# Optimization experiments

Hardware: AMD Instinct MI355X
Metric: run time of the kernel (lower is better)

The kernel has to match this reference:

```python
import jax, jax.numpy as jnp
import numpy as np

L, NH, D, FF, NL, NP = 6, 8, 256, 1024, 4, 4
HD = D // NH
B, Q0 = 4, 1000
SIZES = [(128, 128), (64, 64), (32, 32), (16, 16)]
KEEP_RATIO = 0.5


def _ln(x, w, b, eps=1e-5):
    mu = x.mean(-1, keepdims=True)
    var = ((x - mu) ** 2).mean(-1, keepdims=True)
    return (x - mu) * jax.lax.rsqrt(var + eps) * w + b


def _mha(q, k, v, in_w, in_b, out_w, out_b):
    # torch nn.MultiheadAttention (batch_first, eval mode => no dropout)
    Bq, Qn, _ = q.shape
    wq, wk, wv = jnp.split(in_w, 3, axis=0)
    bq, bk, bv = jnp.split(in_b, 3, axis=0)
    proj = lambda x, w, bb: (x @ w.T + bb).reshape(Bq, -1, NH, HD).transpose(0, 2, 1, 3)
    qh, kh, vh = proj(q, wq, bq), proj(k, wk, bk), proj(v, wv, bv)
    scores = jnp.einsum('bhqd,bhkd->bhqk', qh, kh) * (1.0 / np.float32(np.sqrt(HD)))
    a = jax.nn.softmax(scores, axis=-1)
    o = jnp.einsum('bhqk,bhkd->bhqd', a, vh).transpose(0, 2, 1, 3).reshape(Bq, Qn, D)
    return o @ out_w.T + out_b


def _bilinear(feat, grid):
    # feat [B,NH,HD,H,W]; grid [B,NH,Q,P,2] (x,y) in [-1,1]
    # matches F.grid_sample(mode='bilinear', padding_mode='zeros', align_corners=True)
    Bf, nh, hd, H, W = feat.shape
    gx = (grid[..., 0] + 1.0) * 0.5 * (W - 1)
    gy = (grid[..., 1] + 1.0) * 0.5 * (H - 1)
    x0, y0 = jnp.floor(gx), jnp.floor(gy)
    flat = feat.reshape(Bf, nh, hd, H * W)
    Qn, P = grid.shape[2], grid.shape[3]

    def corner(xi, yi, w):
        valid = (xi >= 0) & (xi <= W - 1) & (yi >= 0) & (yi <= H - 1)
        idx = (jnp.clip(yi, 0, H - 1).astype(jnp.int32) * W
               + jnp.clip(xi, 0, W - 1).astype(jnp.int32)).reshape(Bf, nh, Qn * P)
        vals = jnp.take_along_axis(flat, jnp.broadcast_to(idx[:, :, None, :], (Bf, nh, hd, Qn * P)), axis=3)
        vals = vals.reshape(Bf, nh, hd, Qn, P)
        return vals * (w * valid)[:, :, None]

    wx1, wy1 = gx - x0, gy - y0
    return (corner(x0, y0, (1 - wx1) * (1 - wy1)) + corner(x0 + 1, y0, wx1 * (1 - wy1))
            + corner(x0, y0 + 1, (1 - wx1) * wy1) + corner(x0 + 1, y0 + 1, wx1 * wy1))


def _msdeform(query, feats, ref, off_w, off_b, aw_w, aw_b, out_w, out_b):
    Bq, Qn, _ = query.shape
    off = jnp.tanh((query @ off_w.T + off_b).reshape(Bq, Qn, NH, NL, NP, 2))
    attn = jax.nn.softmax((query @ aw_w.T + aw_b).reshape(Bq, Qn, NH, NL * NP), axis=3)
    attn = attn.reshape(Bq, Qn, NH, NL, NP)
    ref_grid = ref * 2.0 - 1.0  # [B,Q,2]
    agg = 0.0
    for lvl, feat in enumerate(feats):
        fh = feat.reshape(Bq, NH, HD, feat.shape[2], feat.shape[3])
        grid = ref_grid[:, None, :, None, :] + off[:, :, :, lvl].transpose(0, 2, 1, 3, 4)  # [B,NH,Q,NP,2]
        sampled = _bilinear(fh, grid)                     # [B,NH,HD,Q,NP]
        w = attn[:, :, :, lvl].transpose(0, 2, 1, 3)      # [B,NH,Q,NP]
        agg = agg + (sampled * w[:, :, None]).sum(-1)     # [B,NH,HD,Q]
    out = agg.transpose(0, 3, 1, 2).reshape(Bq, Qn, D)
    return out @ out_w.T + out_b, attn


def setup_inputs() -> dict:
    key = jax.random.key(0)
    ks = iter(jax.random.split(key, 64))
    nrm = lambda shape, s=0.02: jax.random.normal(next(ks), shape, jnp.float32) * s
    inp = {
        'query_objects': nrm((B, Q0, D), 1.0),
        'query_embed': nrm((B, Q0, D), 1.0),
    }
    for i, (H, W) in enumerate(SIZES):
        inp[f'feat{i}'] = nrm((B, D, H, W), 1.0)
    inp.update(
        sa_in_w=nrm((L, 3 * D, D)), sa_in_b=jnp.zeros((L, 3 * D)),
        sa_out_w=nrm((L, D, D)), sa_out_b=jnp.zeros((L, D)),
        off_w=nrm((L, NH * NL * NP * 2, D)), off_b=nrm((L, NH * NL * NP * 2), 0.1),
        aw_w=nrm((L, NH * NL * NP, D)), aw_b=jnp.zeros((L, NH * NL * NP)),
        ca_out_w=nrm((L, D, D)), ca_out_b=jnp.zeros((L, D)),
        ff_w1=nrm((L, FF, D)), ff_b1=jnp.zeros((L, FF)),
        ff_w2=nrm((L, D, FF)), ff_b2=jnp.zeros((L, D)),
        nsa_w=jnp.ones((L, D)), nsa_b=jnp.zeros((L, D)),
        nca_w=jnp.ones((L, D)), nca_b=jnp.zeros((L, D)),
        nff_w=jnp.ones((L, D)), nff_b=jnp.zeros((L, D)),
        ref_w1=nrm((D, D)), ref_b1=jnp.zeros((D,)),
        ref_w2=nrm((2, D)), ref_b2=jnp.zeros((2,)),
        score_w=nrm((1, D)), score_b=jnp.zeros((1,)),
        refine_w=nrm((2, D)), refine_b=jnp.zeros((2,)),
    )
    return inp


def reference(query_objects, query_embed, feat0, feat1, feat2, feat3,
              sa_in_w, sa_in_b, sa_out_w, sa_out_b,
              off_w, off_b, aw_w, aw_b, ca_out_w, ca_out_b,
              ff_w1, ff_b1, ff_w2, ff_b2,
              nsa_w, nsa_b, nca_w, nca_b, nff_w, nff_b,
              ref_w1, ref_b1, ref_w2, ref_b2,
              score_w, score_b, refine_w, refine_b):
    feats = [feat0, feat1, feat2, feat3]
    out, q_embed = query_objects, query_embed
    h = jax.nn.relu(q_embed @ ref_w1.T + ref_b1)
    ref_points = jax.nn.sigmoid(h @ ref_w2.T + ref_b2)  # [B,Q,2]
    outputs, attns = [], []
    for i in range(L):
        sa_in = _ln(out, nsa_w[i], nsa_b[i])
        sa_out = _mha(sa_in + q_embed, sa_in + q_embed, sa_in,
                      sa_in_w[i], sa_in_b[i], sa_out_w[i], sa_out_b[i])
        out = out + sa_out
        ca_in = _ln(out, nca_w[i], nca_b[i])
        ca_out, attn = _msdeform(ca_in + q_embed, feats, ref_points,
                                 off_w[i], off_b[i], aw_w[i], aw_b[i], ca_out_w[i], ca_out_b[i])
        out = out + ca_out
        ff_in = _ln(out, nff_w[i], nff_b[i])
        out = out + (jax.nn.relu(ff_in @ ff_w1[i].T + ff_b1[i]) @ ff_w2[i].T + ff_b2[i])
        delta = jnp.tanh(out @ refine_w.T + refine_b) * 0.5
        ref_points = jnp.clip(ref_points + delta, 0.0, 1.0)
        outputs.append(out)
        attns.append(attn)
        if i < L - 1:
            Qn = out.shape[1]
            keep = max(16, int(Qn * KEEP_RATIO))
            scores = jax.nn.sigmoid((jax.lax.stop_gradient(out) @ score_w.T + score_b)[..., 0])
            _, idx = jax.lax.top_k(scores, keep)
            out = jnp.take_along_axis(out, idx[:, :, None], axis=1)
            q_embed = jnp.take_along_axis(q_embed, idx[:, :, None], axis=1)
            ref_points = jnp.take_along_axis(ref_points, idx[:, :, None], axis=1)
    return tuple(outputs) + tuple(attns)
```

## Files before the change

### kernel.cpp

```cpp
#include <hip/hip_runtime.h>
#include <hip/hip_bf16.h>

#define BB 4
#define DD 256

typedef unsigned long long u64;
typedef long long s64;
typedef unsigned int u32;

__device__ __forceinline__ float sigm(float x) { return 1.0f / (1.0f + expf(-x)); }

__global__ void k_ln(const float* __restrict__ x, const float* __restrict__ w,
                     const float* __restrict__ b, float* __restrict__ ln) {
    int row = blockIdx.x, tid = threadIdx.x;
    float v = x[(size_t)row * DD + tid];
    __shared__ float sred[4];
    float s = v;
#pragma unroll
    for (int o = 32; o > 0; o >>= 1) s += __shfl_down(s, o);
    if ((tid & 63) == 0) sred[tid >> 6] = s;
    __syncthreads();
    float mu = (sred[0] + sred[1] + sred[2] + sred[3]) * (1.0f / 256.0f);
    __syncthreads();
    float d = v - mu;
    float s2 = d * d;
#pragma unroll
    for (int o = 32; o > 0; o >>= 1) s2 += __shfl_down(s2, o);
    if ((tid & 63) == 0) sred[tid >> 6] = s2;
    __syncthreads();
    float var = (sred[0] + sred[1] + sred[2] + sred[3]) * (1.0f / 256.0f);
    float r = rsqrtf(var + 1e-5f);
    ln[(size_t)row * DD + tid] = d * r * w[tid] + b[tid];
}

template <int ACT, int RES>
__device__ __forceinline__ void gemm_core(float (*As)[16][64], float (*Ws)[16][64],
                                          const float* __restrict__ A, const float* __restrict__ Pe, int pe,
                                          const float* __restrict__ W, const float* __restrict__ bias,
                                          const float* __restrict__ Rm, float* __restrict__ C,
                                          float* __restrict__ C2,
                                          int M, int N, int K, int row0, int col0) {
    int tid = threadIdx.x;
    int tx = tid & 15, ty = tid >> 4;
    int lm = tid >> 2, lk = (tid & 3) * 4;
    float acc[4][4] = {{0.f}};
    int ar = row0 + lm;
    const float* Arow = A + (size_t)ar * K + lk;
    const float* Prow = pe ? (Pe + (size_t)ar * K + lk) : nullptr;
    const float* Wrow = W + (size_t)(col0 + lm) * K + lk;
    float4 av = make_float4(0.f, 0.f, 0.f, 0.f), wv;
    if (ar < M) {
        av = *(const float4*)(Arow);
        if (pe) { float4 pv = *(const float4*)(Prow); av.x += pv.x; av.y += pv.y; av.z += pv.z; av.w += pv.w; }
    }
    wv = *(const float4*)(Wrow);
    As[0][lk + 0][lm] = av.x; As[0][lk + 1][lm] = av.y; As[0][lk + 2][lm] = av.z; As[0][lk + 3][lm] = av.w;
    Ws[0][lk + 0][lm] = wv.x; Ws[0][lk + 1][lm] = wv.y; Ws[0][lk + 2][lm] = wv.z; Ws[0][lk + 3][lm] = wv.w;
    __syncthreads();
    int nb = K >> 4;
    for (int t = 0; t < nb; t++) {
        int cur = t & 1, nxt = cur ^ 1;
        bool more = (t + 1 < nb);
        if (more) {
            int k0 = (t + 1) << 4;
            av = make_float4(0.f, 0.f, 0.f, 0.f);
            if (ar < M) {
                av = *(const float4*)(Arow + k0);
                if (pe) { float4 pv = *(const float4*)(Prow + k0); av.x += pv.x; av.y += pv.y; av.z += pv.z; av.w += pv.w; }
            }
            wv = *(const float4*)(Wrow + k0);
        }
#pragma unroll
        for (int kk = 0; kk < 16; kk++) {
            float4 a = *(const float4*)&As[cur][kk][ty << 2];
            float4 w = *(const float4*)&Ws[cur][kk][tx << 2];
            acc[0][0] += a.x * w.x; acc[0][1] += a.x * w.y; acc[0][2] += a.x * w.z; acc[0][3] += a.x * w.w;
            acc[1][0] += a.y * w.x; acc[1][1] += a.y * w.y; acc[1][2] += a.y * w.z; acc[1][3] += a.y * w.w;
            acc[2][0] += a.z * w.x; acc[2][1] += a.z * w.y; acc[2][2] += a.z * w.z; acc[2][3] += a.z * w.w;
            acc[3][0] += a.w * w.x; acc[3][1] += a.w * w.y; acc[3][2] += a.w * w.z; acc[3][3] += a.w * w.w;
        }
        if (more) {
            As[nxt][lk + 0][lm] = av.x; As[nxt][lk + 1][lm] = av.y; As[nxt][lk + 2][lm] = av.z; As[nxt][lk + 3][lm] = av.w;
            Ws[nxt][lk + 0][lm] = wv.x; Ws[nxt][lk + 1][lm] = wv.y; Ws[nxt][lk + 2][lm] = wv.z; Ws[nxt][lk + 3][lm] = wv.w;
        }
        __syncthreads();
    }
#pragma unroll
    for (int i2 = 0; i2 < 4; i2++) {
        int r = row0 + (ty << 2) + i2;
        if (r >= M) continue;
        int cc = col0 + (tx << 2);
        float4 v;
        v.x = acc[i2][0] + bias[cc + 0];
        v.y = acc[i2][1] + bias[cc + 1];
        v.z = acc[i2][2] + bias[cc + 2];
        v.w = acc[i2][3] + bias[cc + 3];
        if (ACT == 1) { v.x = fmaxf(v.x, 0.f); v.y = fmaxf(v.y, 0.f); v.z = fmaxf(v.z, 0.f); v.w = fmaxf(v.w, 0.f); }
        if (RES == 1) {
            float4 rm = *(const float4*)(Rm + (size_t)r * N + cc);
            v.x += rm.x; v.y += rm.y; v.z += rm.z; v.w += rm.w;
        }
        *(float4*)(C + (size_t)r * N + cc) = v;
        if (C2) *(float4*)(C2 + (size_t)r * N + cc) = v;
    }
}

template <int ACT, int RES, int PE>
__global__ __launch_bounds__(256) void k_gemm(const float* __restrict__ A, const float* __restrict__ Pe,
                                              const float* __restrict__ W, const float* __restrict__ bias,
                                              const float* __restrict__ Rm, float* __restrict__ C,
                                              int M, int N, int K) {
    __shared__ float As[2][16][64];
    __shared__ float Ws[2][16][64];
    gemm_core<ACT, RES>(As, Ws, A, Pe, PE, W, bias, Rm, C, nullptr, M, N, K, blockIdx.y * 64, blockIdx.x * 64);
}

__global__ __launch_bounds__(256) void k_gemm_st2(const float* __restrict__ A, const float* __restrict__ W,
                                                  const float* __restrict__ bias, const float* __restrict__ Rm,
                                                  float* __restrict__ C, float* __restrict__ C2,
                                                  int M, int N, int K) {
    __shared__ float As[2][16][64];
    __shared__ float Ws[2][16][64];
    gemm_core<0, 1>(As, Ws, A, nullptr, 0, W, bias, Rm, C, C2, M, N, K, blockIdx.y * 64, blockIdx.x * 64);
}

__global__ __launch_bounds__(256) void k_gemm_qkv(const float* __restrict__ A, const float* __restrict__ Pe,
                                                  const float* __restrict__ Wqkv, const float* __restrict__ bqkv,
                                                  float* __restrict__ Cq, float* __restrict__ Ck, float* __restrict__ Cv,
                                                  int M, int K) {
    __shared__ float As[2][16][64];
    __shared__ float Ws[2][16][64];
    int z = blockIdx.z;
    const float* W = Wqkv + (size_t)z * 256 * K;
    const float* bias = bqkv + z * 256;
    float* C = (z == 0) ? Cq : (z == 1) ? Ck : Cv;
    gemm_core<0, 0>(As, Ws, A, Pe, (z < 2) ? 1 : 0, W, bias, nullptr, C, nullptr, M, 256, K,
                    blockIdx.y * 64, blockIdx.x * 64);
}

__global__ __launch_bounds__(256) void k_gemm_offaw(const float* __restrict__ A, const float* __restrict__ Pe,
                                                    const float* __restrict__ Woff, const float* __restrict__ boff,
                                                    const float* __restrict__ Waw, const float* __restrict__ baw,
                                                    float* __restrict__ Coff, float* __restrict__ Caw,
                                                    int M, int K) {
    __shared__ float As[2][16][64];
    __shared__ float Ws[2][16][64];
    int z = blockIdx.z;
    int N = (z == 0) ? 256 : 128;
    if ((int)(blockIdx.x * 64) >= N) return;
    gemm_core<0, 0>(As, Ws, A, Pe, 1, (z == 0) ? Woff : Waw, (z == 0) ? boff : baw, nullptr,
                    (z == 0) ? Coff : Caw, nullptr, M, N, K, blockIdx.y * 64, blockIdx.x * 64);
}

#define MHA_DOT8(SREG, JJ)                                                       \
    {                                                                            \
        _Pragma("unroll")                                                        \
        for (int u = 0; u < 8; u++) SREG[u] = 0.f;                               \
        _Pragma("unroll")                                                        \
        for (int c4 = 0; c4 < 8; c4++) {                                         \
            float q0 = qv[c4 * 4 + 0], q1 = qv[c4 * 4 + 1];                      \
            float q2 = qv[c4 * 4 + 2], q3 = qv[c4 * 4 + 3];                      \
            _Pragma("unroll")                                                    \
            for (int u = 0; u < 8; u++) {                                        \
                float4 k4 = *(const float4*)&Ks[(JJ) + u][c4 * 4];               \
                SREG[u] += q0 * k4.x; SREG[u] += q1 * k4.y;                      \
                SREG[u] += q2 * k4.z; SREG[u] += q3 * k4.w;                      \
            }                                                                    \
        }                                                                        \
    }

__global__ __launch_bounds__(64) void k_qk(const float* __restrict__ Qb, const float* __restrict__ Kb,
                                           float* __restrict__ S, int Qn) {
    int bh = blockIdx.z;
    int b = bh >> 3, h = bh & 7;
    int lane = threadIdx.x;
    int qi = blockIdx.x * 64 + lane;
    int j0 = blockIdx.y * 64;
    __shared__ float Ks[64][36];
    float qv[32];
    const float scale = 0.17677669529663687f;
    bool active = qi < Qn;
    if (active) {
        const float4* qp = (const float4*)(Qb + ((size_t)(b * Qn + qi)) * DD + h * 32);
#pragma unroll
        for (int c4 = 0; c4 < 8; c4++) {
            float4 t = qp[c4];
            qv[c4 * 4 + 0] = t.x * scale; qv[c4 * 4 + 1] = t.y * scale;
            qv[c4 * 4 + 2] = t.z * scale; qv[c4 * 4 + 3] = t.w * scale;
        }
    } else {
#pragma unroll
        for (int c = 0; c < 32; c++) qv[c] = 0.f;
    }
    int nj = Qn - j0; if (nj > 64) nj = 64;
    if (lane < nj) {
        const float4* kp = (const float4*)(Kb + ((size_t)(b * Qn + j0 + lane)) * DD + h * 32);
#pragma unroll
        for (int c4 = 0; c4 < 8; c4++) *(float4*)&Ks[lane][c4 * 4] = kp[c4];
    }
    __syncthreads();
    float* Sp = S + (size_t)bh * Qn * Qn;
    float scur[8];
    for (int g = 0; g < 8; g++) {
        int jj = g << 3;
        if (jj >= nj) break;
        MHA_DOT8(scur, jj)
#pragma unroll
        for (int u = 0; u < 8; u++) {
            int j = j0 + jj + u;
            if (active && j < Qn) Sp[(size_t)j * Qn + qi] = scur[u];
        }
    }
}

__global__ __launch_bounds__(64) void k_mha_s(const float* __restrict__ S, const float* __restrict__ Vb,
                                              float* __restrict__ Ob, int Qn) {
    int bh = blockIdx.y;
    int b = bh >> 3, h = bh & 7;
    int lane = threadIdx.x;
    int qi = blockIdx.x * 64 + lane;
    __shared__ float Vs[64][36];
    float acc[32];
#pragma unroll
    for (int c = 0; c < 32; c++) acc[c] = 0.f;
    float m = -INFINITY, l = 0.f;
    bool active = qi < Qn;
    int qs = active ? qi : 0;
    const float* Sq = S + (size_t)bh * Qn * Qn + qs;
    int ng = Qn >> 3;
    float scur[8], snxt[8];
#pragma unroll
    for (int u = 0; u < 8; u++) scur[u] = Sq[(size_t)u * Qn];
    int gg = 0;
    for (int k0 = 0; k0 < Qn; k0 += 64) {
        int nk = Qn - k0; if (nk > 64) nk = 64;
        if (lane < nk) {
            const float4* vp = (const float4*)(Vb + ((size_t)(b * Qn + k0 + lane)) * DD + h * 32);
#pragma unroll
            for (int c4 = 0; c4 < 8; c4++) *(float4*)&Vs[lane][c4 * 4] = vp[c4];
        }
        __syncthreads();
        int gl = nk >> 3;
        for (int g2 = 0; g2 < gl; g2++, gg++) {
            int jj = g2 << 3;
            bool morep = (gg + 1 < ng);
            if (morep) {
                const float* Sn = Sq + (size_t)(k0 + jj + 8) * Qn;
#pragma unroll
                for (int u = 0; u < 8; u++) snxt[u] = Sn[(size_t)u * Qn];
            }
            float mch[9];
            mch[0] = m;
#pragma unroll
            for (int u = 0; u < 8; u++) mch[u + 1] = fmaxf(mch[u], scur[u]);
            float e8[8];
#pragma unroll
            for (int u = 0; u < 8; u++) e8[u] = expf(fminf(mch[u] - scur[u], scur[u] - mch[u]));
            float sc8[8], p8[8];
#pragma unroll
            for (int u = 0; u < 8; u++) {
                bool gt = scur[u] > mch[u];
                sc8[u] = gt ? e8[u] : 1.0f;
                p8[u] = gt ? 1.0f : e8[u];
                l = l * sc8[u] + p8[u];
            }
            m = mch[8];
            float4 vc[8], vn[8];
#pragma unroll
            for (int c4 = 0; c4 < 8; c4++) vc[c4] = *(const float4*)&Vs[jj][c4 * 4];
#pragma unroll
            for (int u = 0; u < 8; u++) {
                if (u < 7) {
#pragma unroll
                    for (int c4 = 0; c4 < 8; c4++) vn[c4] = *(const float4*)&Vs[jj + u + 1][c4 * 4];
                }
                float sc = sc8[u], p = p8[u];
#pragma unroll
                for (int c4 = 0; c4 < 8; c4++) {
                    acc[c4 * 4 + 0] = acc[c4 * 4 + 0] * sc + p * vc[c4].x;
                    acc[c4 * 4 + 1] = acc[c4 * 4 + 1] * sc + p * vc[c4].y;
                    acc[c4 * 4 + 2] = acc[c4 * 4 + 2] * sc + p * vc[c4].z;
                    acc[c4 * 4 + 3] = acc[c4 * 4 + 3] * sc + p * vc[c4].w;
                }
                if (u < 7) {
#pragma unroll
                    for (int c4 = 0; c4 < 8; c4++) vc[c4] = vn[c4];
                }
            }
            if (morep) {
#pragma unroll
                for (int u = 0; u < 8; u++) scur[u] = snxt[u];
            }
        }
        for (int j = gl << 3; j < nk; j++) {
            float sv = Sq[(size_t)(k0 + j) * Qn];
            float mn = fmaxf(m, sv);
            float e = expf(fminf(m - sv, sv - m));
            bool gt = sv > m;
            float sc = gt ? e : 1.0f;
            float p = gt ? 1.0f : e;
            l = l * sc + p;
            m = mn;
#pragma unroll
            for (int c4 = 0; c4 < 8; c4++) {
                float4 v4 = *(const float4*)&Vs[j][c4 * 4];
                acc[c4 * 4 + 0] = acc[c4 * 4 + 0] * sc + p * v4.x;
                acc[c4 * 4 + 1] = acc[c4 * 4 + 1] * sc + p * v4.y;
                acc[c4 * 4 + 2] = acc[c4 * 4 + 2] * sc + p * v4.z;
                acc[c4 * 4 + 3] = acc[c4 * 4 + 3] * sc + p * v4.w;
            }
        }
        __syncthreads();
    }
    if (active) {
        float inv = 1.0f / l;
        float* op = Ob + ((size_t)(b * Qn + qi)) * DD + h * 32;
#pragma unroll
        for (int c4 = 0; c4 < 8; c4++) {
            float4 o;
            o.x = acc[c4 * 4 + 0] * inv; o.y = acc[c4 * 4 + 1] * inv;
            o.z = acc[c4 * 4 + 2] * inv; o.w = acc[c4 * 4 + 3] * inv;
            *(float4*)(op + c4 * 4) = o;
        }
    }
}

__global__ __launch_bounds__(64) void k_mha(const float* __restrict__ Qb, const float* __restrict__ Kb,
                                            const float* __restrict__ Vb, float* __restrict__ Ob, int Qn) {
    int bh = blockIdx.y;
    int b = bh >> 3, h = bh & 7;
    int lane = threadIdx.x;
    int qi = blockIdx.x * 64 + lane;
    __shared__ float Ks[64][36];
    __shared__ float Vs[64][36];
    float qv[32];
    float acc[32];
#pragma unroll
    for (int c = 0; c < 32; c++) acc[c] = 0.f;
    float m = -INFINITY, l = 0.f;
    const float scale = 0.17677669529663687f;
    bool active = qi < Qn;
    if (active) {
        const float4* qp = (const float4*)(Qb + ((size_t)(b * Qn + qi)) * DD + h * 32);
#pragma unroll
        for (int c4 = 0; c4 < 8; c4++) {
            float4 t = qp[c4];
            qv[c4 * 4 + 0] = t.x * scale; qv[c4 * 4 + 1] = t.y * scale;
            qv[c4 * 4 + 2] = t.z * scale; qv[c4 * 4 + 3] = t.w * scale;
        }
    } else {
#pragma unroll
        for (int c = 0; c < 32; c++) qv[c] = 0.f;
    }
    for (int k0 = 0; k0 < Qn; k0 += 64) {
        int nk = Qn - k0; if (nk > 64) nk = 64;
        if (lane < nk) {
            const float4* kp = (const float4*)(Kb + ((size_t)(b * Qn + k0 + lane)) * DD + h * 32);
            const float4* vp = (const float4*)(Vb + ((size_t)(b * Qn + k0 + lane)) * DD + h * 32);
#pragma unroll
            for (int c4 = 0; c4 < 8; c4++) {
                *(float4*)&Ks[lane][c4 * 4] = kp[c4];
                *(float4*)&Vs[lane][c4 * 4] = vp[c4];
            }
        }
        __syncthreads();
        int ng = nk >> 3;
        float scur[8], snxt[8];
        if (ng > 0) MHA_DOT8(scur, 0)
        for (int g = 0; g < ng; g++) {
            int jj = g << 3;
            bool morep = (g + 1 < ng);
            if (morep) MHA_DOT8(snxt, jj + 8)
            float mch[9];
            mch[0] = m;
#pragma unroll
            for (int u = 0; u < 8; u++) mch[u + 1] = fmaxf(mch[u], scur[u]);
            float e8[8];
#pragma unroll
            for (int u = 0; u < 8; u++) e8[u] = expf(fminf(mch[u] - scur[u], scur[u] - mch[u]));
            float sc8[8], p8[8];
#pragma unroll
            for (int u = 0; u < 8; u++) {
                bool gt = scur[u] > mch[u];
                sc8[u] = gt ? e8[u] : 1.0f;
                p8[u] = gt ? 1.0f : e8[u];
                l = l * sc8[u] + p8[u];
            }
            m = mch[8];
            float4 vc[8], vn[8];
#pragma unroll
            for (int c4 = 0; c4 < 8; c4++) vc[c4] = *(const float4*)&Vs[jj][c4 * 4];
#pragma unroll
            for (int u = 0; u < 8; u++) {
                if (u < 7) {
#pragma unroll
                    for (int c4 = 0; c4 < 8; c4++) vn[c4] = *(const float4*)&Vs[jj + u + 1][c4 * 4];
                }
                float sc = sc8[u], p = p8[u];
#pragma unroll
                for (int c4 = 0; c4 < 8; c4++) {
                    acc[c4 * 4 + 0] = acc[c4 * 4 + 0] * sc + p * vc[c4].x;
                    acc[c4 * 4 + 1] = acc[c4 * 4 + 1] * sc + p * vc[c4].y;
                    acc[c4 * 4 + 2] = acc[c4 * 4 + 2] * sc + p * vc[c4].z;
                    acc[c4 * 4 + 3] = acc[c4 * 4 + 3] * sc + p * vc[c4].w;
                }
                if (u < 7) {
#pragma unroll
                    for (int c4 = 0; c4 < 8; c4++) vc[c4] = vn[c4];
                }
            }
            if (morep) {
#pragma unroll
                for (int u = 0; u < 8; u++) scur[u] = snxt[u];
            }
        }
        for (int j = ng << 3; j < nk; j++) {
            float sv = 0.f;
#pragma unroll
            for (int c4 = 0; c4 < 8; c4++) {
                float4 k4 = *(const float4*)&Ks[j][c4 * 4];
                sv += qv[c4 * 4 + 0] * k4.x; sv += qv[c4 * 4 + 1] * k4.y;
                sv += qv[c4 * 4 + 2] * k4.z; sv += qv[c4 * 4 + 3] * k4.w;
            }
            float mn = fmaxf(m, sv);
            float e = expf(fminf(m - sv, sv - m));
            bool gt = sv > m;
            float sc = gt ? e : 1.0f;
            float p = gt ? 1.0f : e;
            l = l * sc + p;
            m = mn;
#pragma unroll
            for (int c4 = 0; c4 < 8; c4++) {
                float4 v4 = *(const float4*)&Vs[j][c4 * 4];
                acc[c4 * 4 + 0] = acc[c4 * 4 + 0] * sc + p * v4.x;
                acc[c4 * 4 + 1] = acc[c4 * 4 + 1] * sc + p * v4.y;
                acc[c4 * 4 + 2] = acc[c4 * 4 + 2] * sc + p * v4.z;
                acc[c4 * 4 + 3] = acc[c4 * 4 + 3] * sc + p * v4.w;
            }
        }
        __syncthreads();
    }
    if (active) {
        float inv = 1.0f / l;
        float* op = Ob + ((size_t)(b * Qn + qi)) * DD + h * 32;
#pragma unroll
        for (int c4 = 0; c4 < 8; c4++) {
            float4 o;
            o.x = acc[c4 * 4 + 0] * inv; o.y = acc[c4 * 4 + 1] * inv;
            o.z = acc[c4 * 4 + 2] * inv; o.w = acc[c4 * 4 + 3] * inv;
            *(float4*)(op + c4 * 4) = o;
        }
    }
}

__global__ __launch_bounds__(256) void k_trfeat(const float* __restrict__ in, float* __restrict__ out, int HH) {
    __shared__ float t[32][65];
    int bh = blockIdx.y;
    int b = bh >> 3, h = bh & 7;
    int s0 = blockIdx.x * 64;
    int tid = threadIdx.x;
    const float* ip = in + ((size_t)(b * 256 + h * 32)) * HH + s0;
#pragma unroll
    for (int i = 0; i < 8; i++) {
        int idx = i * 256 + tid;
        int c = idx >> 6, s = idx & 63;
        t[c][s] = ip[(size_t)c * HH + s];
    }
    __syncthreads();
    float* op = out + ((size_t)bh * HH + s0) * 32;
#pragma unroll
    for (int i = 0; i < 8; i++) {
        int idx = i * 256 + tid;
        int s = idx >> 5, c = idx & 31;
        op[(size_t)s * 32 + c] = t[c][s];
    }
}

__device__ __forceinline__ float d_samp(const float* fp, int W, int H, int x, int y) {
    if (x < 0 || x > W - 1 || y < 0 || y > H - 1) return 0.f;
    return fp[y * W + x];
}
__device__ __forceinline__ float d_bil(const float* fp, int W, int H, float gx, float gy) {
    float fx = (gx + 1.0f) * 0.5f * (float)(W - 1);
    float fy = (gy + 1.0f) * 0.5f * (float)(H - 1);
    float x0f = floorf(fx), y0f = floorf(fy);
    int x0 = (int)x0f, y0 = (int)y0f;
    float wx = fx - x0f, wy = fy - y0f;
    float v00 = d_samp(fp, W, H, x0, y0);
    float v10 = d_samp(fp, W, H, x0 + 1, y0);
    float v01 = d_samp(fp, W, H, x0, y0 + 1);
    float v11 = d_samp(fp, W, H, x0 + 1, y0 + 1);
    return v00 * (1.f - wx) * (1.f - wy) + v10 * wx * (1.f - wy) + v01 * (1.f - wx) * wy + v11 * wx * wy;
}
__device__ __forceinline__ float d_samp32(const float* fp, int W, int H, int x, int y) {
    if (x < 0 || x > W - 1 || y < 0 || y > H - 1) return 0.f;
    return fp[(size_t)(y * W + x) * 32];
}
__device__ __forceinline__ float d_bil32(const float* fp, int W, int H, float gx, float gy) {
    float fx = (gx + 1.0f) * 0.5f * (float)(W - 1);
    float fy = (gy + 1.0f) * 0.5f * (float)(H - 1);
    float x0f = floorf(fx), y0f = floorf(fy);
    int x0 = (int)x0f, y0 = (int)y0f;
    float wx = fx - x0f, wy = fy - y0f;
    float v00 = d_samp32(fp, W, H, x0, y0);
    float v10 = d_samp32(fp, W, H, x0 + 1, y0);
    float v01 = d_samp32(fp, W, H, x0, y0 + 1);
    float v11 = d_samp32(fp, W, H, x0 + 1, y0 + 1);
    return v00 * (1.f - wx) * (1.f - wy) + v10 * wx * (1.f - wy) + v01 * (1.f - wx) * wy + v11 * wx * wy;
}

template <int TR>
__global__ __launch_bounds__(256) void k_deform(const float* __restrict__ offL, const float* __restrict__ awL,
                                                const float* __restrict__ ref,
                                                const float* __restrict__ f0, const float* __restrict__ f1,
                                                const float* __restrict__ f2, const float* __restrict__ f3,
                                                float* __restrict__ caf, float* __restrict__ attn_out,
                                                int Qn) {
    int row = blockIdx.x;
    int b = row / Qn;
    int tid = threadIdx.x;
    __shared__ float attn_s[8][16];
    __shared__ float off_s[8][16][2];
    __shared__ float rxy[2];
    if (tid < 8) {
        int h = tid;
        const float* ap = awL + (size_t)row * 128 + h * 16;
        float mx = -INFINITY;
        float e[16];
#pragma unroll
        for (int j = 0; j < 16; j++) mx = fmaxf(mx, ap[j]);
        float ssum = 0.f;
#pragma unroll
        for (int j = 0; j < 16; j++) { e[j] = expf(ap[j] - mx); ssum += e[j]; }
        float inv = 1.0f / ssum;
        float* ao = attn_out + (size_t)row * 128 + h * 16;
#pragma unroll
        for (int j = 0; j < 16; j++) {
            float p = e[j] * inv;
            attn_s[h][j] = p;
            ao[j] = p;
        }
        const float* op = offL + (size_t)row * 256 + h * 32;
#pragma unroll
        for (int j = 0; j < 16; j++) {
            off_s[h][j][0] = tanhf(op[j * 2 + 0]);
            off_s[h][j][1] = tanhf(op[j * 2 + 1]);
        }
    }
    if (tid == 8) {
        rxy[0] = ref[(size_t)row * 2 + 0] * 2.f - 1.f;
        rxy[1] = ref[(size_t)row * 2 + 1] * 2.f - 1.f;
    }
    __syncthreads();
    int h = tid >> 5, c = tid & 31;
    float agg = 0.f;
#pragma unroll
    for (int l = 0; l < 4; l++) {
        const int H = 128 >> l;
        const float* base = (l == 0 ? f0 : l == 1 ? f1 : l == 2 ? f2 : f3);
        const float* fp;
        if (TR) fp = base + ((size_t)(b * 8 + h) * (H * H)) * 32 + c;
        else    fp = base + (size_t)(b * DD + h * 32 + c) * H * H;
#pragma unroll
        for (int p = 0; p < 4; p++) {
            int j = l * 4 + p;
            float sv;
            if (TR) sv = d_bil32(fp, H, H, rxy[0] + off_s[h][j][0], rxy[1] + off_s[h][j][1]);
            else    sv = d_bil(fp, H, H, rxy[0] + off_s[h][j][0], rxy[1] + off_s[h][j][1]);
            agg += attn_s[h][j] * sv;
        }
    }
    caf[(size_t)row * DD + h * 32 + c] = agg;
}

__global__ __launch_bounds__(64) void k_refinit(const float* __restrict__ hbuf, const float* __restrict__ w2,
                                                const float* __restrict__ b2, float* __restrict__ ref) {
    int row = blockIdx.x, lane = threadIdx.x;
    const float* hp = hbuf + (size_t)row * DD;
    float s0 = 0.f, s1 = 0.f;
#pragma unroll
    for (int d = 0; d < 4; d++) {
        int dd = lane + d * 64;
        float v = hp[dd];
        s0 += v * w2[dd];
        s1 += v * w2[DD + dd];
    }
#pragma unroll
    for (int o = 32; o > 0; o >>= 1) { s0 += __shfl_down(s0, o); s1 += __shfl_down(s1, o); }
    if (lane == 0) {
        ref[(size_t)row * 2 + 0] = sigm(s0 + b2[0]);
        ref[(size_t)row * 2 + 1] = sigm(s1 + b2[1]);
    }
}

__global__ __launch_bounds__(64) void k_refsc(const float* __restrict__ out, const float* __restrict__ rw,
                                              const float* __restrict__ rb, float* __restrict__ ref,
                                              const float* __restrict__ sw, const float* __restrict__ sb,
                                              float* __restrict__ score) {
    int row = blockIdx.x, lane = threadIdx.x;
    const float* op = out + (size_t)row * DD;
    float s0 = 0.f, s1 = 0.f;
#pragma unroll
    for (int d = 0; d < 4; d++) {
        int dd = lane + d * 64;
        float v = op[dd];
        s0 += v * rw[dd];
        s1 += v * rw[DD + dd];
    }
#pragma unroll
    for (int o = 32; o > 0; o >>= 1) { s0 += __shfl_down(s0, o); s1 += __shfl_down(s1, o); }
    if (lane == 0) {
        float r0 = ref[(size_t)row * 2 + 0] + tanhf(s0 + rb[0]) * 0.5f;
        float r1 = ref[(size_t)row * 2 + 1] + tanhf(s1 + rb[1]) * 0.5f;
        ref[(size_t)row * 2 + 0] = fminf(fmaxf(r0, 0.f), 1.f);
        ref[(size_t)row * 2 + 1] = fminf(fmaxf(r1, 0.f), 1.f);
        float s = sb[0];
        for (int d = 0; d < DD; d++) s += op[d] * sw[d];
        score[row] = sigm(s);
    }
}

__global__ __launch_bounds__(256) void k_topk(const float* __restrict__ score, int* __restrict__ idx,
                                              int Qn, int PAD, int keep) {
    __shared__ u64 keys[1024];
    int b = blockIdx.x, tid = threadIdx.x;
    for (int q = tid; q < PAD; q += 256) {
        u64 key;
        if (q < Qn) {
            u32 u = __float_as_uint(score[b * Qn + q]);
            u = (u & 0x80000000u) ? ~u : (u | 0x80000000u);
            u32 hi = ~u;
            key = (((u64)hi) << 32) | (u32)q;
        } else {
            key = 0xFFFFFFFFFFFFFFFFULL;
        }
        keys[q] = key;
    }
    __syncthreads();
    for (int k = 2; k <= PAD; k <<= 1) {
        for (int j = k >> 1; j > 0; j >>= 1) {
            for (int i = tid; i < PAD; i += 256) {
                int ij = i ^ j;
                if (ij > i) {
                    bool up = ((i & k) == 0);
                    u64 a = keys[i], c = keys[ij];
                    if ((a > c) == up) { keys[i] = c; keys[ij] = a; }
                }
            }
            __syncthreads();
        }
    }
    for (int t = tid; t < keep; t += 256) idx[b * keep + t] = (int)(keys[t] & 0xFFFFFFFFu);
}

__global__ __launch_bounds__(256) void k_gather(const float* __restrict__ osrc, const float* __restrict__ esrc,
                                                const float* __restrict__ rsrc, const int* __restrict__ idx,
                                                float* __restrict__ oT, float* __restrict__ eT,
                                                float* __restrict__ rT, int Qin, int keep) {
    int j = blockIdx.x;
    int b = j / keep;
    int src = idx[j];
    int tid = threadIdx.x;
    size_t srow = (size_t)(b * Qin + src), drow = (size_t)j;
    oT[drow * DD + tid] = osrc[srow * DD + tid];
    eT[drow * DD + tid] = esrc[srow * DD + tid];
    if (tid < 2) rT[drow * 2 + tid] = rsrc[srow * 2 + tid];
}

__global__ __launch_bounds__(256) void k_copyback(const float* __restrict__ oT, const float* __restrict__ eT,
                                                  const float* __restrict__ rT, float* __restrict__ o,
                                                  float* __restrict__ e, float* __restrict__ r) {
    int row = blockIdx.x, tid = threadIdx.x;
    o[(size_t)row * DD + tid] = oT[(size_t)row * DD + tid];
    e[(size_t)row * DD + tid] = eT[(size_t)row * DD + tid];
    if (tid < 2) r[(size_t)row * 2 + tid] = rT[(size_t)row * 2 + tid];
}

extern "C" void kernel_launch(void* const* d_in, const int* in_sizes, int n_in,
                              void* d_out, int out_size, void* d_ws, size_t ws_size,
                              hipStream_t stream) {
    (void)in_sizes; (void)n_in; (void)out_size;
    const float* q_obj = (const float*)d_in[0];
    const float* q_emb = (const float*)d_in[1];
    const float* feat0 = (const float*)d_in[2];
    const float* feat1 = (const float*)d_in[3];
    const float* feat2 = (const float*)d_in[4];
    const float* feat3 = (const float*)d_in[5];
    const float* sa_in_w = (const float*)d_in[6];
    const float* sa_in_b = (const float*)d_in[7];
    const float* sa_out_w = (const float*)d_in[8];
    const float* sa_out_b = (const float*)d_in[9];
    const float* off_w = (const float*)d_in[10];
    const float* off_b = (const float*)d_in[11];
    const float* aw_w = (const float*)d_in[12];
    const float* aw_b = (const float*)d_in[13];
    const float* ca_out_w = (const float*)d_in[14];
    const float* ca_out_b = (const float*)d_in[15];
    const float* ff_w1 = (const float*)d_in[16];
    const float* ff_b1 = (const float*)d_in[17];
    const float* ff_w2 = (const float*)d_in[18];
    const float* ff_b2 = (const float*)d_in[19];
    const float* nsa_w = (const float*)d_in[20];
    const float* nsa_b = (const float*)d_in[21];
    const float* nca_w = (const float*)d_in[22];
    const float* nca_b = (const float*)d_in[23];
    const float* nff_w = (const float*)d_in[24];
    const float* nff_b = (const float*)d_in[25];
    const float* ref_w1 = (const float*)d_in[26];
    const float* ref_b1 = (const float*)d_in[27];
    const float* ref_w2 = (const float*)d_in[28];
    const float* ref_b2 = (const float*)d_in[29];
    const float* score_w = (const float*)d_in[30];
    const float* score_b = (const float*)d_in[31];
    const float* refine_w = (const float*)d_in[32];
    const float* refine_b = (const float*)d_in[33];

    float* outf = (float*)d_out;
    float* ws = (float*)d_ws;
    const int RD = 4000 * 256;
    float* f_out = ws;
    float* f_emb = ws + RD;
    float* f_ln  = ws + 2 * RD;
    float* sc0   = ws + 3 * RD;
    float* sc1   = ws + 4 * RD;
    float* sc2   = ws + 5 * RD;
    float* f_ref = ws + 6 * RD;
    float* f_sc  = ws + 6 * RD + 8000;
    int*   i_idx = (int*)(ws + 6 * RD + 12032);
    float* f_tr  = ws + 6 * RD + 16384;
    static const s64 tr_ofs[4] = {0, 16777216, 20971520, 22020096};
    const size_t tr_need_bytes = ((size_t)(6 * RD + 16384) + 22282240ULL) * 4ULL;
    const bool use_tr = ws_size >= tr_need_bytes;
    float* Sbuf   = f_tr + 22282240;
    float* f_hid  = Sbuf + 32000000;
    float* f_out2 = f_hid + 4096000;
    float* f_emb2 = f_out2 + 1024000;
    float* f_ref2 = f_emb2 + 1024000;
    const size_t ext_need_bytes = ((size_t)28442624ULL + 32000000ULL + 4096000ULL + 1024000ULL + 1024000ULL + 8000ULL) * 4ULL;
    const bool use_ext = use_tr && (ws_size >= ext_need_bytes);

    static const int Qs[6] = {1000, 500, 250, 125, 62, 31};
    static const s64 out_ofs[6] = {0, 1024000, 1536000, 1792000, 1920000, 1983488};
    static const s64 attn_ofs[6] = {2015232, 2527232, 2783232, 2911232, 2975232, 3006976};

    hipMemcpyAsync(f_out, q_obj, (size_t)RD * 4, hipMemcpyDeviceToDevice, stream);
    hipMemcpyAsync(f_emb, q_emb, (size_t)RD * 4, hipMemcpyDeviceToDevice, stream);

    if (use_tr) {
        k_trfeat<<<dim3(16384 / 64, 32), 256, 0, stream>>>(feat0, f_tr + tr_ofs[0], 16384);
        k_trfeat<<<dim3(4096 / 64, 32), 256, 0, stream>>>(feat1, f_tr + tr_ofs[1], 4096);
        k_trfeat<<<dim3(1024 / 64, 32), 256, 0, stream>>>(feat2, f_tr + tr_ofs[2], 1024);
        k_trfeat<<<dim3(256 / 64, 32), 256, 0, stream>>>(feat3, f_tr + tr_ofs[3], 256);
    }

    k_gemm<1, 0, 0><<<dim3(4, 63), 256, 0, stream>>>(f_emb, nullptr, ref_w1, ref_b1, nullptr, f_ln, 4000, 256, 256);
    k_refinit<<<4000, 64, 0, stream>>>(f_ln, ref_w2, ref_b2, f_ref);

    float* po = f_out; float* pe = f_emb; float* pr = f_ref;
    float* qo = f_out2; float* qe = f_emb2; float* qr = f_ref2;

    for (int i = 0; i < 6; i++) {
        const int Q = Qs[i];
        const int R = BB * Q;
        const int gy = (R + 63) / 64;
        const float* siw = sa_in_w + (size_t)i * 768 * 256;
        const float* sib = sa_in_b + (size_t)i * 768;

        k_ln<<<R, 256, 0, stream>>>(po, nsa_w + i * 256, nsa_b + i * 256, f_ln);
        k_gemm_qkv<<<dim3(4, gy, 3), 256, 0, stream>>>(f_ln, pe, siw, sib, sc0, sc1, sc2, R, 256);
        if (use_ext) {
            int qt = (Q + 63) / 64;
            k_qk<<<dim3(qt, qt, 32), 64, 0, stream>>>(sc0, sc1, Sbuf, Q);
            k_mha_s<<<dim3(qt, 32), 64, 0, stream>>>(Sbuf, sc2, f_ln, Q);
        } else {
            k_mha<<<dim3((Q + 63) / 64, 32), 64, 0, stream>>>(sc0, sc1, sc2, f_ln, Q);
        }
        k_gemm<0, 1, 0><<<dim3(4, gy), 256, 0, stream>>>(f_ln, nullptr, sa_out_w + (size_t)i * 65536,
                                                         sa_out_b + i * 256, po, po, R, 256, 256);

        k_ln<<<R, 256, 0, stream>>>(po, nca_w + i * 256, nca_b + i * 256, f_ln);
        k_gemm_offaw<<<dim3(4, gy, 2), 256, 0, stream>>>(f_ln, pe, off_w + (size_t)i * 65536, off_b + i * 256,
                                                         aw_w + (size_t)i * 32768, aw_b + i * 128, sc0, sc1, R, 256);
        if (use_tr)
            k_deform<1><<<R, 256, 0, stream>>>(sc0, sc1, pr, f_tr + tr_ofs[0], f_tr + tr_ofs[1],
                                               f_tr + tr_ofs[2], f_tr + tr_ofs[3], sc2, outf + attn_ofs[i], Q);
        else
            k_deform<0><<<R, 256, 0, stream>>>(sc0, sc1, pr, feat0, feat1, feat2, feat3, sc2,
                                               outf + attn_ofs[i], Q);
        k_gemm<0, 1, 0><<<dim3(4, gy), 256, 0, stream>>>(sc2, nullptr, ca_out_w + (size_t)i * 65536,
                                                         ca_out_b + i * 256, po, po, R, 256, 256);

        k_ln<<<R, 256, 0, stream>>>(po, nff_w + i * 256, nff_b + i * 256, f_ln);
        if (use_ext) {
            k_gemm<1, 0, 0><<<dim3(16, gy), 256, 0, stream>>>(f_ln, nullptr,
                                                              ff_w1 + (size_t)i * 262144, ff_b1 + i * 1024,
                                                              nullptr, f_hid, R, 1024, 256);
            k_gemm_st2<<<dim3(4, gy), 256, 0, stream>>>(f_hid, ff_w2 + (size_t)i * 262144,
                                                        ff_b2 + i * 256, po, po,
                                                        outf + out_ofs[i], R, 256, 1024);
        } else {
            for (int r0 = 0; r0 < R; r0 += 2000) {
                int mc = R - r0; if (mc > 2000) mc = 2000;
                int gyc = (mc + 63) / 64;
                k_gemm<1, 0, 0><<<dim3(16, gyc), 256, 0, stream>>>(f_ln + (size_t)r0 * 256, nullptr,
                                                                   ff_w1 + (size_t)i * 262144, ff_b1 + i * 1024,
                                                                   nullptr, sc0, mc, 1024, 256);
                k_gemm_st2<<<dim3(4, gyc), 256, 0, stream>>>(sc0, ff_w2 + (size_t)i * 262144,
                                                             ff_b2 + i * 256, po + (size_t)r0 * 256,
                                                             po + (size_t)r0 * 256,
                                                             outf + out_ofs[i] + (size_t)r0 * 256, mc, 256, 1024);
            }
        }

        if (i < 5) {
            int keep = Qs[i + 1];
            int PAD = 1;
            while (PAD < Q) PAD <<= 1;
            k_refsc<<<R, 64, 0, stream>>>(po, refine_w, refine_b, pr, score_w, score_b, f_sc);
            k_topk<<<4, 256, 0, stream>>>(f_sc, i_idx, Q, PAD, keep);
            if (use_ext) {
                k_gather<<<4 * keep, 256, 0, stream>>>(po, pe, pr, i_idx, qo, qe, qr, Q, keep);
                float* t;
                t = po; po = qo; qo = t;
                t = pe; pe = qe; qe = t;
                t = pr; pr = qr; qr = t;
            } else {
                k_gather<<<4 * keep, 256, 0, stream>>>(po, pe, pr, i_idx, sc0, sc1, sc2, Q, keep);
                k_copyback<<<4 * keep, 256, 0, stream>>>(sc0, sc1, sc2, po, pe, pr);
            }
        }
    }
}
```

Measured before the change: 2.117 ms.

## Pipeline softmax stats one group ahead in MHA and add 8x8-register FF1 GEMM

The MHA softmax-V kernel now computes the online-softmax scale and probability factors for the next 8-key group while the current group's V accumulation runs. It also prefetches scores two groups ahead, so the exp chain overlaps the FMA work. Separately, the first feed-forward GEMM gets a dedicated 64-thread kernel with an 8x8 per-thread register tile, fused bias and ReLU, used on the ext path. The changes add register pressure and reduce threads per block, which could hurt occupancy.

```diff
diff --git a/kernel.cpp b/kernel.cpp
--- a/kernel.cpp
+++ b/kernel.cpp
@@ -152,6 +152,88 @@
                     (z == 0) ? Coff : Caw, nullptr, M, N, K, blockIdx.y * 64, blockIdx.x * 64);
 }
 
+__global__ __launch_bounds__(64) void k_ff1(const float* __restrict__ A, const float* __restrict__ W,
+                                            const float* __restrict__ bias, float* __restrict__ C, int M) {
+    const int K = 256;
+    __shared__ float As[2][16][64];
+    __shared__ float Ws[2][16][64];
+    int tid = threadIdx.x;
+    int tx = tid & 7, ty = tid >> 3;
+    int row0 = blockIdx.y * 64, col0 = blockIdx.x * 64;
+    int ar = row0 + tid;
+    const float* Arow = A + (size_t)ar * K;
+    const float* Wrow = W + (size_t)(col0 + tid) * K;
+    float acc[8][8] = {{0.f}};
+    float4 a4[4], w4[4];
+#pragma unroll
+    for (int q = 0; q < 4; q++) {
+        a4[q] = (ar < M) ? *(const float4*)(Arow + q * 4) : make_float4(0.f, 0.f, 0.f, 0.f);
+        w4[q] = *(const float4*)(Wrow + q * 4);
+    }
+#pragma unroll
+    for (int q = 0; q < 4; q++) {
+        As[0][q * 4 + 0][tid] = a4[q].x; As[0][q * 4 + 1][tid] = a4[q].y;
+        As[0][q * 4 + 2][tid] = a4[q].z; As[0][q * 4 + 3][tid] = a4[q].w;
+        Ws[0][q * 4 + 0][tid] = w4[q].x; Ws[0][q * 4 + 1][tid] = w4[q].y;
+        Ws[0][q * 4 + 2][tid] = w4[q].z; Ws[0][q * 4 + 3][tid] = w4[q].w;
+    }
+    __syncthreads();
+    const int nb = K >> 4;
+    for (int t = 0; t < nb; t++) {
+        int cur = t & 1, nxt = cur ^ 1;
+        bool more = (t + 1 < nb);
+        if (more) {
+            int k0 = (t + 1) << 4;
+#pragma unroll
+            for (int q = 0; q < 4; q++) {
+                a4[q] = (ar < M) ? *(const float4*)(Arow + k0 + q * 4) : make_float4(0.f, 0.f, 0.f, 0.f);
+                w4[q] = *(const float4*)(Wrow + k0 + q * 4);
+            }
+        }
+#pragma unroll
+        for (int kk = 0; kk < 16; kk++) {
+            float4 xa0 = *(const float4*)&As[cur][kk][ty * 8];
+            float4 xa1 = *(const float4*)&As[cur][kk][ty * 8 + 4];
+            float4 xw0 = *(const float4*)&Ws[cur][kk][tx * 8];
+            float4 xw1 = *(const float4*)&Ws[cur][kk][tx * 8 + 4];
+            float av8[8] = {xa0.x, xa0.y, xa0.z, xa0.w, xa1.x, xa1.y, xa1.z, xa1.w};
+            float wv8[8] = {xw0.x, xw0.y, xw0.z, xw0.w, xw1.x, xw1.y, xw1.z, xw1.w};
+#pragma unroll
+            for (int i = 0; i < 8; i++)
+#pragma unroll
+                for (int j2 = 0; j2 < 8; j2++)
+                    acc[i][j2] += av8[i] * wv8[j2];
+        }
+        if (more) {
+#pragma unroll
+            for (int q = 0; q < 4; q++) {
+                As[nxt][q * 4 + 0][tid] = a4[q].x; As[nxt][q * 4 + 1][tid] = a4[q].y;
+                As[nxt][q * 4 + 2][tid] = a4[q].z; As[nxt][q * 4 + 3][tid] = a4[q].w;
+                Ws[nxt][q * 4 + 0][tid] = w4[q].x; Ws[nxt][q * 4 + 1][tid] = w4[q].y;
+                Ws[nxt][q * 4 + 2][tid] = w4[q].z; Ws[nxt][q * 4 + 3][tid] = w4[q].w;
+            }
+        }
+        __syncthreads();
+    }
+#pragma unroll
+    for (int i = 0; i < 8; i++) {
+        int r = row0 + ty * 8 + i;
+        if (r >= M) continue;
+        int cc = col0 + tx * 8;
+        float4 v0, v1;
+        v0.x = fmaxf(acc[i][0] + bias[cc + 0], 0.f);
+        v0.y = fmaxf(acc[i][1] + bias[cc + 1], 0.f);
+        v0.z = fmaxf(acc[i][2] + bias[cc + 2], 0.f);
+        v0.w = fmaxf(acc[i][3] + bias[cc + 3], 0.f);
+        v1.x = fmaxf(acc[i][4] + bias[cc + 4], 0.f);
+        v1.y = fmaxf(acc[i][5] + bias[cc + 5], 0.f);
+        v1.z = fmaxf(acc[i][6] + bias[cc + 6], 0.f);
+        v1.w = fmaxf(acc[i][7] + bias[cc + 7], 0.f);
+        *(float4*)(C + (size_t)r * 1024 + cc) = v0;
+        *(float4*)(C + (size_t)r * 1024 + cc + 4) = v1;
+    }
+}
+
 #define MHA_DOT8(SREG, JJ)                                                       \
     {                                                                            \
         _Pragma("unroll")                                                        \
@@ -169,6 +251,26 @@
         }                                                                        \
     }
 
+#define MHA_AB(SARR, SCARR, PARR)                                                \
+    {                                                                            \
+        float mch[9];                                                            \
+        mch[0] = m;                                                              \
+        _Pragma("unroll")                                                        \
+        for (int u = 0; u < 8; u++) mch[u + 1] = fmaxf(mch[u], SARR[u]);         \
+        float e8[8];                                                             \
+        _Pragma("unroll")                                                        \
+        for (int u = 0; u < 8; u++)                                              \
+            e8[u] = expf(fminf(mch[u] - SARR[u], SARR[u] - mch[u]));             \
+        _Pragma("unroll")                                                        \
+        for (int u = 0; u < 8; u++) {                                            \
+            bool gt = SARR[u] > mch[u];                                          \
+            SCARR[u] = gt ? e8[u] : 1.0f;                                        \
+            PARR[u] = gt ? 1.0f : e8[u];                                         \
+            l = l * SCARR[u] + PARR[u];                                          \
+        }                                                                        \
+        m = mch[8];                                                              \
+    }
+
 __global__ __launch_bounds__(64) void k_qk(const float* __restrict__ Qb, const float* __restrict__ Kb,
                                            float* __restrict__ S, int Qn) {
     int bh = blockIdx.z;
@@ -228,9 +330,18 @@
     int qs = active ? qi : 0;
     const float* Sq = S + (size_t)bh * Qn * Qn + qs;
     int ng = Qn >> 3;
-    float scur[8], snxt[8];
-#pragma unroll
-    for (int u = 0; u < 8; u++) scur[u] = Sq[(size_t)u * Qn];
+    float sc8c[8], p8c[8], sc8n[8], p8n[8];
+    float snxt[8] = {0.f}, snn[8] = {0.f};
+    {
+        float s0b[8];
+#pragma unroll
+        for (int u = 0; u < 8; u++) s0b[u] = Sq[(size_t)u * Qn];
+        if (ng > 1) {
+#pragma unroll
+            for (int u = 0; u < 8; u++) snxt[u] = Sq[(size_t)(8 + u) * Qn];
+        }
+        MHA_AB(s0b, sc8c, p8c)
+    }
     int gg = 0;
     for (int k0 = 0; k0 < Qn; k0 += 64) {
         int nk = Qn - k0; if (nk > 64) nk = 64;
@@ -243,38 +354,25 @@
         int gl = nk >> 3;
         for (int g2 = 0; g2 < gl; g2++, gg++) {
             int jj = g2 << 3;
-            bool morep = (gg + 1 < ng);
-            if (morep) {
-                const float* Sn = Sq + (size_t)(k0 + jj + 8) * Qn;
-#pragma unroll
-                for (int u = 0; u < 8; u++) snxt[u] = Sn[(size_t)u * Qn];
-            }
-            float mch[9];
-            mch[0] = m;
-#pragma unroll
-            for (int u = 0; u < 8; u++) mch[u + 1] = fmaxf(mch[u], scur[u]);
-            float e8[8];
-#pragma unroll
-            for (int u = 0; u < 8; u++) e8[u] = expf(fminf(mch[u] - scur[u], scur[u] - mch[u]));
-            float sc8[8], p8[8];
-#pragma unroll
-            for (int u = 0; u < 8; u++) {
-                bool gt = scur[u] > mch[u];
-                sc8[u] = gt ? e8[u] : 1.0f;
-                p8[u] = gt ? 1.0f : e8[u];
-                l = l * sc8[u] + p8[u];
-            }
-            m = mch[8];
-            float4 vc[8], vn[8];
+            float4 vc[8];
 #pragma unroll
             for (int c4 = 0; c4 < 8; c4++) vc[c4] = *(const float4*)&Vs[jj][c4 * 4];
+            bool have2 = (gg + 2) < ng;
+            if (have2) {
+                const float* Sn = Sq + (size_t)((gg + 2) << 3) * Qn;
+#pragma unroll
+                for (int u = 0; u < 8; u++) snn[u] = Sn[(size_t)u * Qn];
+            }
+            bool morep = (gg + 1) < ng;
+            if (morep) MHA_AB(snxt, sc8n, p8n)
+            float4 vn[8];
 #pragma unroll
             for (int u = 0; u < 8; u++) {
                 if (u < 7) {
 #pragma unroll
                     for (int c4 = 0; c4 < 8; c4++) vn[c4] = *(const float4*)&Vs[jj + u + 1][c4 * 4];
                 }
-                float sc = sc8[u], p = p8[u];
+                float sc = sc8c[u], p = p8c[u];
 #pragma unroll
                 for (int c4 = 0; c4 < 8; c4++) {
                     acc[c4 * 4 + 0] = acc[c4 * 4 + 0] * sc + p * vc[c4].x;
@@ -289,7 +387,11 @@
             }
             if (morep) {
 #pragma unroll
-                for (int u = 0; u < 8; u++) scur[u] = snxt[u];
+                for (int u = 0; u < 8; u++) {
+                    snxt[u] = snn[u];
+                    sc8c[u] = sc8n[u];
+                    p8c[u] = p8n[u];
+                }
             }
         }
         for (int j = gl << 3; j < nk; j++) {
@@ -366,27 +468,13 @@
         __syncthreads();
         int ng = nk >> 3;
         float scur[8], snxt[8];
+        float sc8[8], p8[8];
         if (ng > 0) MHA_DOT8(scur, 0)
         for (int g = 0; g < ng; g++) {
             int jj = g << 3;
             bool morep = (g + 1 < ng);
             if (morep) MHA_DOT8(snxt, jj + 8)
-            float mch[9];
-            mch[0] = m;
-#pragma unroll
-            for (int u = 0; u < 8; u++) mch[u + 1] = fmaxf(mch[u], scur[u]);
-            float e8[8];
-#pragma unroll
-            for (int u = 0; u < 8; u++) e8[u] = expf(fminf(mch[u] - scur[u], scur[u] - mch[u]));
-            float sc8[8], p8[8];
-#pragma unroll
-            for (int u = 0; u < 8; u++) {
-                bool gt = scur[u] > mch[u];
-                sc8[u] = gt ? e8[u] : 1.0f;
-                p8[u] = gt ? 1.0f : e8[u];
-                l = l * sc8[u] + p8[u];
-            }
-            m = mch[8];
+            MHA_AB(scur, sc8, p8)
             float4 vc[8], vn[8];
 #pragma unroll
             for (int c4 = 0; c4 < 8; c4++) vc[c4] = *(const float4*)&Vs[jj][c4 * 4];
@@ -792,9 +880,8 @@
 
         k_ln<<<R, 256, 0, stream>>>(po, nff_w + i * 256, nff_b + i * 256, f_ln);
         if (use_ext) {
-            k_gemm<1, 0, 0><<<dim3(16, gy), 256, 0, stream>>>(f_ln, nullptr,
-                                                              ff_w1 + (size_t)i * 262144, ff_b1 + i * 1024,
-                                                              nullptr, f_hid, R, 1024, 256);
+            k_ff1<<<dim3(16, gy), 64, 0, stream>>>(f_ln, ff_w1 + (size_t)i * 262144, ff_b1 + i * 1024,
+                                                   f_hid, R);
             k_gemm_st2<<<dim3(4, gy), 256, 0, stream>>>(f_hid, ff_w2 + (size_t)i * 262144,
                                                         ff_b2 + i * 256, po, po,
                                                         outf + out_ofs[i], R, 256, 1024);
```

Measured after the change: 2.275 ms. 1.07x slower.
